# Kernel optimization log

Measured on AMD Instinct MI355X. Metric: run time of the kernel, lower is better.

The kernel has to match this reference:

```python
import jax, jax.numpy as jnp
import numpy as np

EPS = 1e-05


def setup_inputs() -> dict:
    key = jax.random.key(0)
    ks = jax.random.split(key, 7)
    T, d = 8192, 512
    h = jax.random.normal(ks[0], (T, d), dtype=jnp.float32)
    ln_w = jax.random.normal(ks[1], (d,), dtype=jnp.float32) * 0.1
    ln_b = jax.random.normal(ks[2], (d,), dtype=jnp.float32) * 0.1
    w_q = jax.random.normal(ks[3], (d, d), dtype=jnp.float32) * 0.1
    w_k = jax.random.normal(ks[4], (d, d), dtype=jnp.float32) * 0.1
    w_v = jax.random.normal(ks[5], (d, d), dtype=jnp.float32) * 0.1
    w_o = jax.random.normal(ks[6], (d, d), dtype=jnp.float32) * 0.1
    return {"h": h, "ln_w": ln_w, "ln_b": ln_b,
            "w_q": w_q, "w_k": w_k, "w_v": w_v, "w_o": w_o}


def reference(h, ln_w, ln_b, w_q, w_k, w_v, w_o):
    T, d = h.shape
    # LayerNorm (biased variance, matching torch)
    mu = jnp.mean(h, axis=-1, keepdims=True)
    var = jnp.mean(jnp.square(h - mu), axis=-1, keepdims=True)
    h_norm = (h - mu) * jax.lax.rsqrt(var + EPS) * ln_w + ln_b
    # nn.Linear applies x @ W.T
    q = h_norm @ w_q.T  # [T, d]
    k = h_norm @ w_k.T
    v = h_norm @ w_v.T
    scores = (q @ k.T) * (1.0 / jnp.sqrt(jnp.float32(d)))  # [T, T]
    causal = jnp.tril(jnp.ones((T, T), dtype=bool))
    scores = jnp.where(causal, scores, -jnp.inf)
    attn = jax.nn.softmax(scores, axis=-1)
    out = (attn @ v) @ w_o.T
    return h + out
```

## Files before the change

### kernel.cpp

```cpp
#include <hip/hip_runtime.h>
#include <stdint.h>

#define T_SEQ 8192
#define DMODEL 512
#define QKV_LD 1536

typedef __attribute__((ext_vector_type(8))) short bfx8;
typedef __attribute__((ext_vector_type(4))) short bfx4;
typedef __attribute__((ext_vector_type(4))) float fx4;
typedef __attribute__((ext_vector_type(16))) float f32x16;

__device__ __forceinline__ unsigned short f2bf(float f) {
    uint32_t u = __float_as_uint(f);
    u += 0x7fffu + ((u >> 16) & 1u);
    return (unsigned short)(u >> 16);
}
__device__ __forceinline__ float bf2f(unsigned short s) {
    return __uint_as_float(((uint32_t)s) << 16);
}

__device__ __forceinline__ void gload16(const void* g, void* l) {
    __builtin_amdgcn_global_load_lds(
        (const __attribute__((address_space(1))) unsigned int*)g,
        (__attribute__((address_space(3))) unsigned int*)l,
        16, 0, 0);
}

__device__ __forceinline__ void fence_barrier() {
    asm volatile("" ::: "memory");
    __builtin_amdgcn_s_barrier();
    asm volatile("" ::: "memory");
}

__global__ __launch_bounds__(256) void cvt_bf16_kernel(const float* __restrict__ src,
                                                       unsigned short* __restrict__ dst, int n) {
    int i = (blockIdx.x * 256 + threadIdx.x) * 8;
    if (i >= n) return;
    fx4 a = *(const fx4*)(src + i);
    fx4 b = *(const fx4*)(src + i + 4);
    bfx8 o;
    o[0] = f2bf(a[0]); o[1] = f2bf(a[1]); o[2] = f2bf(a[2]); o[3] = f2bf(a[3]);
    o[4] = f2bf(b[0]); o[5] = f2bf(b[1]); o[6] = f2bf(b[2]); o[7] = f2bf(b[3]);
    *(bfx8*)(dst + i) = o;
}

__global__ __launch_bounds__(256) void layernorm_kernel(const float* __restrict__ h,
                                                        const float* __restrict__ w,
                                                        const float* __restrict__ b,
                                                        unsigned short* __restrict__ out) {
    int wv = threadIdx.x >> 6, lane = threadIdx.x & 63;
    int row = blockIdx.x * 4 + wv;
    const float* hr = h + (size_t)row * DMODEL + lane * 8;
    fx4 x0 = *(const fx4*)hr;
    fx4 x1 = *(const fx4*)(hr + 4);
    float s  = x0[0]+x0[1]+x0[2]+x0[3]+x1[0]+x1[1]+x1[2]+x1[3];
    float ss = x0[0]*x0[0]+x0[1]*x0[1]+x0[2]*x0[2]+x0[3]*x0[3]
             + x1[0]*x1[0]+x1[1]*x1[1]+x1[2]*x1[2]+x1[3]*x1[3];
    #pragma unroll
    for (int m = 1; m < 64; m <<= 1) { s += __shfl_xor(s, m); ss += __shfl_xor(ss, m); }
    float mu  = s * (1.0f / DMODEL);
    float var = ss * (1.0f / DMODEL) - mu * mu;
    float r = rsqrtf(var + 1e-5f);
    const float* wp = w + lane * 8; const float* bp = b + lane * 8;
    fx4 w0 = *(const fx4*)wp, w1 = *(const fx4*)(wp + 4);
    fx4 b0 = *(const fx4*)bp, b1 = *(const fx4*)(bp + 4);
    bfx8 o;
    o[0] = f2bf((x0[0]-mu)*r*w0[0] + b0[0]);
    o[1] = f2bf((x0[1]-mu)*r*w0[1] + b0[1]);
    o[2] = f2bf((x0[2]-mu)*r*w0[2] + b0[2]);
    o[3] = f2bf((x0[3]-mu)*r*w0[3] + b0[3]);
    o[4] = f2bf((x1[0]-mu)*r*w1[0] + b1[0]);
    o[5] = f2bf((x1[1]-mu)*r*w1[1] + b1[1]);
    o[6] = f2bf((x1[2]-mu)*r*w1[2] + b1[2]);
    o[7] = f2bf((x1[3]-mu)*r*w1[3] + b1[3]);
    *(bfx8*)(out + (size_t)row * DMODEL + lane * 8) = o;
}

template<int RESID>
__global__ __launch_bounds__(256, 2) void gemm_bt_kernel(
    const unsigned short* __restrict__ A,
    const unsigned short* __restrict__ B,
    unsigned short* __restrict__ Cb,
    float* __restrict__ Cf,
    const float* __restrict__ resid,
    int M, int N, int K)
{
    __shared__ unsigned short At[128 * 64];
    __shared__ unsigned short Bt[128 * 64];
    int tid = threadIdx.x;
    int wv = tid >> 6, lane = tid & 63, l15 = lane & 15, l4 = lane >> 4;
    int wr = wv >> 1, wc = wv & 1;
    int row0 = blockIdx.y * 128;
    int col0 = blockIdx.x * 128;
    fx4 acc[4][4] = {};
    const char* Abase = (const char*)(A + (size_t)row0 * K);
    const char* Bbase = (const char*)(B + (size_t)col0 * K);
    for (int kt = 0; kt < K; kt += 64) {
        #pragma unroll
        for (int ch = 0; ch < 4; ch++) {
            int bix = (ch * 256 + tid) * 16;
            int r = bix >> 7;
            int sb = (bix & 127) ^ ((r & 7) << 4);
            bfx8 va = *(const bfx8*)(Abase + (size_t)r * (K * 2) + kt * 2 + sb);
            bfx8 vb = *(const bfx8*)(Bbase + (size_t)r * (K * 2) + kt * 2 + sb);
            *(bfx8*)((char*)At + bix) = va;
            *(bfx8*)((char*)Bt + bix) = vb;
        }
        __syncthreads();
        #pragma unroll
        for (int ks = 0; ks < 2; ks++) {
            bfx8 af[4], bf[4];
            #pragma unroll
            for (int m = 0; m < 4; m++) {
                int ra = wr * 64 + m * 16 + l15;
                int ka = (ks * 64 + l4 * 16) ^ ((ra & 7) << 4);
                af[m] = *(const bfx8*)((const char*)At + ra * 128 + ka);
                int rb = wc * 64 + m * 16 + l15;
                int kb = (ks * 64 + l4 * 16) ^ ((rb & 7) << 4);
                bf[m] = *(const bfx8*)((const char*)Bt + rb * 128 + kb);
            }
            #pragma unroll
            for (int m = 0; m < 4; m++)
                #pragma unroll
                for (int n = 0; n < 4; n++)
                    acc[m][n] = __builtin_amdgcn_mfma_f32_16x16x32_bf16(af[m], bf[n], acc[m][n], 0, 0, 0);
        }
        __syncthreads();
    }
    #pragma unroll
    for (int m = 0; m < 4; m++)
        #pragma unroll
        for (int n = 0; n < 4; n++)
            #pragma unroll
            for (int r = 0; r < 4; r++) {
                int row = row0 + wr * 64 + m * 16 + l4 * 4 + r;
                int col = col0 + wc * 64 + n * 16 + l15;
                float v = acc[m][n][r];
                size_t o = (size_t)row * N + col;
                if (RESID) Cf[o] = v + resid[o];
                else       Cb[o] = f2bf(v);
            }
}

__global__ __launch_bounds__(256) void transpose_kernel(const unsigned short* __restrict__ v,
                                                        unsigned short* __restrict__ vt, int ld) {
    __shared__ unsigned short tile[64][80];
    int t = threadIdx.x;
    int r0 = blockIdx.x * 64;
    int c0 = blockIdx.y * 64;
    int r = t >> 2, cw = (t & 3) * 16;
    const unsigned short* src = v + (size_t)(r0 + r) * ld + c0 + cw;
    bfx8 a = *(const bfx8*)src;
    bfx8 b = *(const bfx8*)(src + 8);
    #pragma unroll
    for (int j = 0; j < 8; j++) { tile[r][cw + j] = a[j]; tile[r][cw + 8 + j] = b[j]; }
    __syncthreads();
    int dc = t >> 2, rb = (t & 3) * 16;
    bfx8 o0, o1;
    #pragma unroll
    for (int j = 0; j < 8; j++) { o0[j] = tile[rb + j][dc]; o1[j] = tile[rb + 8 + j][dc]; }
    unsigned short* dst = vt + (size_t)(c0 + dc) * T_SEQ + r0 + rb;
    *(bfx8*)dst = o0;
    *(bfx8*)(dst + 8) = o1;
}

__global__ __launch_bounds__(768)
void flash9_kernel(
    const unsigned short* __restrict__ q,
    const unsigned short* __restrict__ k,
    const unsigned short* __restrict__ vt,
    unsigned short* __restrict__ opart,
    float* __restrict__ mbuf, float* __restrict__ lbuf,
    int CH, int NBLK)
{
    __shared__ unsigned short Q_lds[64 * 512];
    __shared__ unsigned short K_lds[32 * 512];
    __shared__ unsigned short V_lds[512 * 32];
    __shared__ unsigned short Sp_lds[2 * 64 * 32];
    __shared__ unsigned short p_lds[64 * 32];
    __shared__ float alpha_lds[64];

    int tid = threadIdx.x;
    int wv = tid >> 6, lane = tid & 63, l15 = lane & 15, l4 = lane >> 4;
    int l31 = lane & 31, hi = lane >> 5;
    bool isS = wv < 4;

    int L = blockIdx.x;
    int bid = (L & 7) * (NBLK >> 3) + (L >> 3);

    int c = 0;
    while (bid >= 128 * (c + 1) - CH * (c + 1) * c / 2) c++;
    int qi = CH * c + (bid - (128 * c - CH * c * (c - 1) / 2));
    int R0 = qi * 64;
    int kv_begin = c * CH * 64;
    int kv_end = min(kv_begin + CH * 64, R0 + 64);
    int ntile = (kv_end - kv_begin) >> 5;

    int qg = wv >> 1, kb = wv & 1;
    int ro = (wv - 4) >> 2, co = (wv - 4) & 3;

    const float rscale = 0.044194173824159216f;

    float m_run = -INFINITY, l_run = 0.f;
    int srow = wv * 16 + (lane >> 2);
    fx4 acc[2][8] = {};

    auto stageQ = [&]() {
        if (wv >= 8) return;
        const char* qb = (const char*)q + (size_t)R0 * (QKV_LD * 2);
        #pragma unroll
        for (int j = 0; j < 8; j++) {
            int row = wv * 8 + j;
            const char* gp = qb + (size_t)row * (QKV_LD * 2)
                           + ((lane * 16) ^ ((row & 15) << 4));
            gload16(gp, (char*)Q_lds + row * 1024);
        }
    };
    auto stageK2 = [&](int kv0) {
        if (wv >= 8) return;
        const char* kbp = (const char*)k + (size_t)kv0 * (QKV_LD * 2);
        #pragma unroll
        for (int j = 0; j < 4; j++) {
            int row = wv * 4 + j;
            const char* gp = kbp + (size_t)row * (QKV_LD * 2)
                           + ((lane * 16) ^ ((row & 15) << 4));
            gload16(gp, (char*)K_lds + row * 1024);
        }
    };
    auto stageV2 = [&](int kv0) {
        if (wv < 4) return;
        const char* vb = (const char*)vt + (size_t)kv0 * 2;
        #pragma unroll
        for (int j = 0; j < 4; j++) {
            int seg = (wv - 4) * 4 + j;
            int dr = seg * 16 + (lane >> 2);
            const char* gp = vb + (size_t)dr * (T_SEQ * 2)
                           + (((lane & 3) * 16) ^ ((dr & 3) << 4));
            gload16(gp, (char*)V_lds + seg * 1024);
        }
    };

    stageQ();
    stageK2(kv_begin);

    for (int t = 0; t <= ntile; t++) {
        int kv0 = kv_begin + t * 32;

        asm volatile("s_waitcnt vmcnt(0)" ::: "memory");
        fence_barrier();
        __builtin_amdgcn_sched_barrier(0);

        if (isS) {
            if (t < ntile) {
                f32x16 sacc = {};
                int ksw = (l31 & 15) << 4;
                int qrow = qg * 32 + l31;
                int qsw = (qrow & 15) << 4;
                const char* kbase = (const char*)K_lds + l31 * 1024;
                const char* qbase = (const char*)Q_lds + qrow * 1024;
                #pragma unroll
                for (int ks = 0; ks < 16; ks++) {
                    int off = kb * 512 + ks * 32 + hi * 16;
                    bfx8 kfr = *(const bfx8*)(kbase + (off ^ ksw));
                    bfx8 qfr = *(const bfx8*)(qbase + (off ^ qsw));
                    sacc = __builtin_amdgcn_mfma_f32_32x32x16_bf16(kfr, qfr, sacc, 0, 0, 0);
                }
                char* spb = (char*)Sp_lds + kb * 4096 + qrow * 64;
                int spsw = (qrow & 3) << 4;
                #pragma unroll
                for (int a = 0; a < 4; a++) {
                    bfx4 ch;
                    #pragma unroll
                    for (int b = 0; b < 4; b++) {
                        int r = a * 4 + b;
                        int kvloc = b + 8 * a + 4 * hi;
                        float x = sacc[r] * rscale;
                        if (kv0 + kvloc > R0 + qrow) x = -INFINITY;
                        ch[b] = (short)f2bf(x);
                    }
                    *(bfx4*)(spb + ((a * 16 + hi * 8) ^ spsw)) = ch;
                }
            }
        } else {
            if (t > 0) {
                fx4 apv[2];
                apv[0] = *(const fx4*)&alpha_lds[ro * 32 + l4 * 4];
                apv[1] = *(const fx4*)&alpha_lds[ro * 32 + 16 + l4 * 4];
                #pragma unroll
                for (int m = 0; m < 2; m++)
                    #pragma unroll
                    for (int n = 0; n < 8; n++)
                        #pragma unroll
                        for (int r = 0; r < 4; r++)
                            acc[m][n][r] *= apv[m][r];
                bfx8 pa[2];
                #pragma unroll
                for (int m = 0; m < 2; m++) {
                    int prow = ro * 32 + m * 16 + l15;
                    pa[m] = *(const bfx8*)((const char*)p_lds + prow * 64
                                           + ((l4 * 16) ^ ((prow & 3) << 4)));
                }
                #pragma unroll
                for (int n = 0; n < 8; n++) {
                    int d = co * 128 + n * 16 + l15;
                    bfx8 vfr = *(const bfx8*)((const char*)V_lds + (size_t)d * 64
                                              + ((l4 * 16) ^ ((d & 3) << 4)));
                    acc[0][n] = __builtin_amdgcn_mfma_f32_16x16x32_bf16(pa[0], vfr, acc[0][n], 0, 0, 0);
                    acc[1][n] = __builtin_amdgcn_mfma_f32_16x16x32_bf16(pa[1], vfr, acc[1][n], 0, 0, 0);
                }
            }
        }
        if (t == ntile) break;

        asm volatile("s_waitcnt lgkmcnt(0)" ::: "memory");
        fence_barrier();
        __builtin_amdgcn_sched_barrier(0);

        if (t + 1 < ntile) stageK2(kv0 + 32);
        stageV2(kv0);

        if (isS) {
            int soff = srow * 64 + (((lane & 3) * 16) ^ ((srow & 3) << 4));
            bfx8 s0 = *(const bfx8*)((const char*)Sp_lds + soff);
            bfx8 s1 = *(const bfx8*)((const char*)Sp_lds + 4096 + soff);
            float xv[8];
            float mx = -INFINITY;
            #pragma unroll
            for (int j = 0; j < 8; j++) {
                xv[j] = bf2f((unsigned short)s0[j]) + bf2f((unsigned short)s1[j]);
                mx = fmaxf(mx, xv[j]);
            }
            mx = fmaxf(mx, __shfl_xor(mx, 1));
            mx = fmaxf(mx, __shfl_xor(mx, 2));
            float mn = fmaxf(m_run, mx);
            float msafe = (mn == -INFINITY) ? 0.f : mn;
            float al = __expf(m_run - msafe);
            m_run = mn;
            if ((lane & 3) == 0) alpha_lds[srow] = al;
            float ps = 0.f;
            bfx8 pw;
            #pragma unroll
            for (int j = 0; j < 8; j++) {
                float p = __expf(xv[j] - msafe);
                pw[j] = (short)f2bf(p);
                ps += p;
            }
            *(bfx8*)((char*)p_lds + soff) = pw;
            ps += __shfl_xor(ps, 1);
            ps += __shfl_xor(ps, 2);
            l_run = l_run * al + ps;
        }
    }

    if (!isS) {
        #pragma unroll
        for (int m = 0; m < 2; m++)
            #pragma unroll
            for (int n = 0; n < 8; n++)
                #pragma unroll
                for (int r = 0; r < 4; r++) {
                    int rowl = ro * 32 + m * 16 + l4 * 4 + r;
                    int col = co * 128 + n * 16 + l15;
                    opart[((size_t)bid * 64 + rowl) * DMODEL + col] = f2bf(acc[m][n][r]);
                }
    } else if ((lane & 3) == 0) {
        mbuf[(size_t)bid * 64 + srow] = m_run;
        lbuf[(size_t)bid * 64 + srow] = l_run;
    }
}

__global__ __launch_bounds__(256) void combine2_kernel(
    const unsigned short* __restrict__ opart,
    const float* __restrict__ mbuf, const float* __restrict__ lbuf,
    unsigned short* __restrict__ attn, int CH)
{
    int tid = threadIdx.x;
    int row = blockIdx.x * 4 + (tid >> 6);
    int col = (tid & 63) * 8;
    int qi = row >> 6, rowl = row & 63;
    int nch = qi / CH + 1;
    float M = -INFINITY;
    for (int c = 0; c < nch; c++) {
        int pidx = 128 * c - CH * c * (c - 1) / 2 + (qi - CH * c);
        M = fmaxf(M, mbuf[(size_t)pidx * 64 + rowl]);
    }
    float L = 0.f;
    float accv[8] = {0.f,0.f,0.f,0.f,0.f,0.f,0.f,0.f};
    for (int c = 0; c < nch; c++) {
        int pidx = 128 * c - CH * c * (c - 1) / 2 + (qi - CH * c);
        float e = __expf(mbuf[(size_t)pidx * 64 + rowl] - M);
        L += lbuf[(size_t)pidx * 64 + rowl] * e;
        bfx8 v = *(const bfx8*)(opart + ((size_t)pidx * 64 + rowl) * DMODEL + col);
        #pragma unroll
        for (int j = 0; j < 8; j++) accv[j] += e * bf2f((unsigned short)v[j]);
    }
    float invL = 1.0f / L;
    bfx8 o;
    #pragma unroll
    for (int j = 0; j < 8; j++) o[j] = f2bf(accv[j] * invL);
    *(bfx8*)(attn + (size_t)row * DMODEL + col) = o;
}

extern "C" void kernel_launch(void* const* d_in, const int* in_sizes, int n_in,
                              void* d_out, int out_size, void* d_ws, size_t ws_size,
                              hipStream_t stream) {
    const float* h   = (const float*)d_in[0];
    const float* lnw = (const float*)d_in[1];
    const float* lnb = (const float*)d_in[2];
    const float* wq  = (const float*)d_in[3];
    const float* wk  = (const float*)d_in[4];
    const float* wv  = (const float*)d_in[5];
    const float* wo  = (const float*)d_in[6];
    float* out = (float*)d_out;

    char* ws = (char*)d_ws;
    size_t off = 0;
    auto alloc = [&](size_t bytes) {
        char* p = ws + off;
        off += (bytes + 255) & ~(size_t)255;
        return p;
    };
    const size_t TD2 = (size_t)T_SEQ * DMODEL * 2;
    const size_t W2  = (size_t)DMODEL * DMODEL * 2;
    unsigned short* hn   = (unsigned short*)alloc(TD2);
    unsigned short* wqkv = (unsigned short*)alloc(3 * W2);
    unsigned short* wob  = (unsigned short*)alloc(W2);
    unsigned short* qkvb = (unsigned short*)alloc((size_t)T_SEQ * QKV_LD * 2);
    unsigned short* vtb  = (unsigned short*)alloc(TD2);
    unsigned short* attnb= (unsigned short*)alloc(TD2);

    int CH = 8, NBLK = 1088;
    {
        size_t need = off + 2 * ((1088u * 64 * 4 + 255) & ~(size_t)255)
                    + (((size_t)1088 * 64 * 512 * 2 + 255) & ~(size_t)255);
        if (need > ws_size) { CH = 16; NBLK = 576; }
    }
    float* mbuf = (float*)alloc((size_t)NBLK * 64 * 4);
    float* lbuf = (float*)alloc((size_t)NBLK * 64 * 4);
    unsigned short* opart = (unsigned short*)alloc((size_t)NBLK * 64 * 512 * 2);

    cvt_bf16_kernel<<<dim3(128), dim3(256), 0, stream>>>(wq, wqkv,                   DMODEL * DMODEL);
    cvt_bf16_kernel<<<dim3(128), dim3(256), 0, stream>>>(wk, wqkv + DMODEL*DMODEL,   DMODEL * DMODEL);
    cvt_bf16_kernel<<<dim3(128), dim3(256), 0, stream>>>(wv, wqkv + 2*DMODEL*DMODEL, DMODEL * DMODEL);
    cvt_bf16_kernel<<<dim3(128), dim3(256), 0, stream>>>(wo, wob, DMODEL * DMODEL);

    layernorm_kernel<<<dim3(T_SEQ / 4), dim3(256), 0, stream>>>(h, lnw, lnb, hn);

    gemm_bt_kernel<0><<<dim3(QKV_LD / 128, T_SEQ / 128), dim3(256), 0, stream>>>(
        hn, wqkv, qkvb, nullptr, nullptr, T_SEQ, QKV_LD, DMODEL);

    transpose_kernel<<<dim3(T_SEQ / 64, DMODEL / 64), dim3(256), 0, stream>>>(
        qkvb + 2 * DMODEL, vtb, QKV_LD);

    flash9_kernel<<<dim3(NBLK), dim3(768), 0, stream>>>(
        qkvb, qkvb + DMODEL, vtb, opart, mbuf, lbuf, CH, NBLK);

    combine2_kernel<<<dim3(T_SEQ / 4), dim3(256), 0, stream>>>(opart, mbuf, lbuf, attnb, CH);

    gemm_bt_kernel<1><<<dim3(DMODEL / 128, T_SEQ / 128), dim3(256), 0, stream>>>(
        attnb, wob, nullptr, out, h, T_SEQ, DMODEL, DMODEL);
}
```

Baseline: 261.9 us.

## Move online softmax into PV waves with double-buffered score tiles

Takes the online-softmax step (row max, exp, running sum and rescale factor) out of the score waves and runs it inside the PV waves. Each PV wave reads raw scores from a double-buffered score LDS array, computes P in registers and broadcasts alpha by shuffle. This drops the p_lds and alpha_lds round trips and the serial softmax phase between barriers. The QK^T loop also splits into two independent MFMA accumulator chains to shorten dependency stalls. The cost is redundant softmax work across the four column-group PV waves, plus extra registers and shuffles in those waves.

```diff
diff --git a/kernel.cpp b/kernel.cpp
--- a/kernel.cpp
+++ b/kernel.cpp
@@ -165,7 +165,7 @@
 }
 
 __global__ __launch_bounds__(768)
-void flash9_kernel(
+void flash11_kernel(
     const unsigned short* __restrict__ q,
     const unsigned short* __restrict__ k,
     const unsigned short* __restrict__ vt,
@@ -176,9 +176,7 @@
     __shared__ unsigned short Q_lds[64 * 512];
     __shared__ unsigned short K_lds[32 * 512];
     __shared__ unsigned short V_lds[512 * 32];
-    __shared__ unsigned short Sp_lds[2 * 64 * 32];
-    __shared__ unsigned short p_lds[64 * 32];
-    __shared__ float alpha_lds[64];
+    __shared__ unsigned short Sp_lds[2][2][64 * 32];
 
     int tid = threadIdx.x;
     int wv = tid >> 6, lane = tid & 63, l15 = lane & 15, l4 = lane >> 4;
@@ -201,8 +199,8 @@
 
     const float rscale = 0.044194173824159216f;
 
-    float m_run = -INFINITY, l_run = 0.f;
-    int srow = wv * 16 + (lane >> 2);
+    float m_run[2] = { -INFINITY, -INFINITY };
+    float l_run[2] = { 0.f, 0.f };
     fx4 acc[2][8] = {};
 
     auto stageQ = [&]() {
@@ -252,20 +250,24 @@
 
         if (isS) {
             if (t < ntile) {
-                f32x16 sacc = {};
+                f32x16 sa0 = {}, sa1 = {};
                 int ksw = (l31 & 15) << 4;
                 int qrow = qg * 32 + l31;
                 int qsw = (qrow & 15) << 4;
                 const char* kbase = (const char*)K_lds + l31 * 1024;
                 const char* qbase = (const char*)Q_lds + qrow * 1024;
                 #pragma unroll
-                for (int ks = 0; ks < 16; ks++) {
-                    int off = kb * 512 + ks * 32 + hi * 16;
-                    bfx8 kfr = *(const bfx8*)(kbase + (off ^ ksw));
-                    bfx8 qfr = *(const bfx8*)(qbase + (off ^ qsw));
-                    sacc = __builtin_amdgcn_mfma_f32_32x32x16_bf16(kfr, qfr, sacc, 0, 0, 0);
-                }
-                char* spb = (char*)Sp_lds + kb * 4096 + qrow * 64;
+                for (int ks = 0; ks < 16; ks += 2) {
+                    int off0 = kb * 512 + ks * 32 + hi * 16;
+                    int off1 = off0 + 32;
+                    bfx8 k0 = *(const bfx8*)(kbase + (off0 ^ ksw));
+                    bfx8 q0 = *(const bfx8*)(qbase + (off0 ^ qsw));
+                    bfx8 k1 = *(const bfx8*)(kbase + (off1 ^ ksw));
+                    bfx8 q1 = *(const bfx8*)(qbase + (off1 ^ qsw));
+                    sa0 = __builtin_amdgcn_mfma_f32_32x32x16_bf16(k0, q0, sa0, 0, 0, 0);
+                    sa1 = __builtin_amdgcn_mfma_f32_32x32x16_bf16(k1, q1, sa1, 0, 0, 0);
+                }
+                char* spb = (char*)&Sp_lds[t & 1][kb][0] + qrow * 64;
                 int spsw = (qrow & 3) << 4;
                 #pragma unroll
                 for (int a = 0; a < 4; a++) {
@@ -274,7 +276,7 @@
                     for (int b = 0; b < 4; b++) {
                         int r = a * 4 + b;
                         int kvloc = b + 8 * a + 4 * hi;
-                        float x = sacc[r] * rscale;
+                        float x = (sa0[r] + sa1[r]) * rscale;
                         if (kv0 + kvloc > R0 + qrow) x = -INFINITY;
                         ch[b] = (short)f2bf(x);
                     }
@@ -283,22 +285,56 @@
             }
         } else {
             if (t > 0) {
-                fx4 apv[2];
-                apv[0] = *(const fx4*)&alpha_lds[ro * 32 + l4 * 4];
-                apv[1] = *(const fx4*)&alpha_lds[ro * 32 + 16 + l4 * 4];
-                #pragma unroll
-                for (int m = 0; m < 2; m++)
+                int t1 = (t - 1) & 1;
+                float xv[2][8];
+                float mx[2];
+                #pragma unroll
+                for (int m = 0; m < 2; m++) {
+                    int row = ro * 32 + m * 16 + l15;
+                    int soff = row * 64 + ((l4 * 16) ^ ((row & 3) << 4));
+                    bfx8 s0 = *(const bfx8*)((const char*)&Sp_lds[t1][0][0] + soff);
+                    bfx8 s1 = *(const bfx8*)((const char*)&Sp_lds[t1][1][0] + soff);
+                    mx[m] = -INFINITY;
                     #pragma unroll
-                    for (int n = 0; n < 8; n++)
-                        #pragma unroll
-                        for (int r = 0; r < 4; r++)
-                            acc[m][n][r] *= apv[m][r];
+                    for (int j = 0; j < 8; j++) {
+                        xv[m][j] = bf2f((unsigned short)s0[j]) + bf2f((unsigned short)s1[j]);
+                        mx[m] = fmaxf(mx[m], xv[m][j]);
+                    }
+                    mx[m] = fmaxf(mx[m], __shfl_xor(mx[m], 16));
+                    mx[m] = fmaxf(mx[m], __shfl_xor(mx[m], 32));
+                }
+                float al[2];
                 bfx8 pa[2];
                 #pragma unroll
                 for (int m = 0; m < 2; m++) {
-                    int prow = ro * 32 + m * 16 + l15;
-                    pa[m] = *(const bfx8*)((const char*)p_lds + prow * 64
-                                           + ((l4 * 16) ^ ((prow & 3) << 4)));
+                    float mn = fmaxf(m_run[m], mx[m]);
+                    float msafe = (mn == -INFINITY) ? 0.f : mn;
+                    al[m] = __expf(m_run[m] - msafe);
+                    m_run[m] = mn;
+                    float rs = 0.f;
+                    #pragma unroll
+                    for (int j = 0; j < 8; j++) {
+                        float p = __expf(xv[m][j] - msafe);
+                        pa[m][j] = (short)f2bf(p);
+                        rs += p;
+                    }
+                    rs += __shfl_xor(rs, 16);
+                    rs += __shfl_xor(rs, 32);
+                    l_run[m] = l_run[m] * al[m] + rs;
+                }
+                #pragma unroll
+                for (int m = 0; m < 2; m++) {
+                    float a0 = __shfl(al[m], l4 * 4 + 0);
+                    float a1 = __shfl(al[m], l4 * 4 + 1);
+                    float a2 = __shfl(al[m], l4 * 4 + 2);
+                    float a3 = __shfl(al[m], l4 * 4 + 3);
+                    #pragma unroll
+                    for (int n = 0; n < 8; n++) {
+                        acc[m][n][0] *= a0;
+                        acc[m][n][1] *= a1;
+                        acc[m][n][2] *= a2;
+                        acc[m][n][3] *= a3;
+                    }
                 }
                 #pragma unroll
                 for (int n = 0; n < 8; n++) {
@@ -318,38 +354,6 @@
 
         if (t + 1 < ntile) stageK2(kv0 + 32);
         stageV2(kv0);
-
-        if (isS) {
-            int soff = srow * 64 + (((lane & 3) * 16) ^ ((srow & 3) << 4));
-            bfx8 s0 = *(const bfx8*)((const char*)Sp_lds + soff);
-            bfx8 s1 = *(const bfx8*)((const char*)Sp_lds + 4096 + soff);
-            float xv[8];
-            float mx = -INFINITY;
-            #pragma unroll
-            for (int j = 0; j < 8; j++) {
-                xv[j] = bf2f((unsigned short)s0[j]) + bf2f((unsigned short)s1[j]);
-                mx = fmaxf(mx, xv[j]);
-            }
-            mx = fmaxf(mx, __shfl_xor(mx, 1));
-            mx = fmaxf(mx, __shfl_xor(mx, 2));
-            float mn = fmaxf(m_run, mx);
-            float msafe = (mn == -INFINITY) ? 0.f : mn;
-            float al = __expf(m_run - msafe);
-            m_run = mn;
-            if ((lane & 3) == 0) alpha_lds[srow] = al;
-            float ps = 0.f;
-            bfx8 pw;
-            #pragma unroll
-            for (int j = 0; j < 8; j++) {
-                float p = __expf(xv[j] - msafe);
-                pw[j] = (short)f2bf(p);
-                ps += p;
-            }
-            *(bfx8*)((char*)p_lds + soff) = pw;
-            ps += __shfl_xor(ps, 1);
-            ps += __shfl_xor(ps, 2);
-            l_run = l_run * al + ps;
-        }
     }
 
     if (!isS) {
@@ -363,9 +367,14 @@
                     int col = co * 128 + n * 16 + l15;
                     opart[((size_t)bid * 64 + rowl) * DMODEL + col] = f2bf(acc[m][n][r]);
                 }
-    } else if ((lane & 3) == 0) {
-        mbuf[(size_t)bid * 64 + srow] = m_run;
-        lbuf[(size_t)bid * 64 + srow] = l_run;
+        if (co == 0 && l4 == 0) {
+            #pragma unroll
+            for (int m = 0; m < 2; m++) {
+                int rowl = ro * 32 + m * 16 + l15;
+                mbuf[(size_t)bid * 64 + rowl] = m_run[m];
+                lbuf[(size_t)bid * 64 + rowl] = l_run[m];
+            }
+        }
     }
 }
 
@@ -452,7 +461,7 @@
     transpose_kernel<<<dim3(T_SEQ / 64, DMODEL / 64), dim3(256), 0, stream>>>(
         qkvb + 2 * DMODEL, vtb, QKV_LD);
 
-    flash9_kernel<<<dim3(NBLK), dim3(768), 0, stream>>>(
+    flash11_kernel<<<dim3(NBLK), dim3(768), 0, stream>>>(
         qkvb, qkvb + DMODEL, vtb, opart, mbuf, lbuf, CH, NBLK);
 
     combine2_kernel<<<dim3(T_SEQ / 4), dim3(256), 0, stream>>>(opart, mbuf, lbuf, attnb, CH);
```

Result: slower. 383.0 us (+46.2%).
